# Performance work log

Hardware: AMD Instinct MI355X
Metric: run time of the kernel (lower is better)

Reference implementation:

```python
import jax, jax.numpy as jnp
import numpy as np
import math
from jax import lax

B, C, L = 8, 512, 1024
NCONV, K, H = 4, 7, 8
DH = C // H
EPS = 1e-5
NEG = -1e30


def layer_norm(x, g, b):
    mu = jnp.mean(x, axis=-1, keepdims=True)
    var = jnp.mean(jnp.square(x - mu), axis=-1, keepdims=True)
    return (x - mu) * lax.rsqrt(var + EPS) * g + b


def positional_encoding(d, n):
    pos = jnp.arange(n, dtype=jnp.float32)[:, None]                     # [n,1]
    div = jnp.exp(jnp.arange(0, d, 2, dtype=jnp.float32) * (-math.log(10000.0) / d))
    ang = pos * div                                                      # [n,d/2]
    pe = jnp.zeros((d, n), dtype=jnp.float32)
    pe = pe.at[0::2].set(jnp.sin(ang).T).at[1::2].set(jnp.cos(ang).T)
    return pe                                                            # [d,n]


def setup_inputs() -> dict:
    key = jax.random.key(0)
    ks = jax.random.split(key, 20)
    s = 0.02
    inp = {
        "x": jax.random.normal(ks[0], (B, C, L), jnp.float32),
        "mask": jnp.ones((B, L), jnp.float32),
        # conv stack params (stacked over NCONV layers)
        "dw_w": jax.random.normal(ks[1], (NCONV, C, 1, K), jnp.float32) * s,
        "dw_b": jnp.zeros((NCONV, C), jnp.float32),
        "pw_w": jax.random.normal(ks[2], (NCONV, C, C), jnp.float32) * s,
        "pw_b": jnp.zeros((NCONV, C), jnp.float32),
        "ln_conv_g": jnp.ones((NCONV, C), jnp.float32),
        "ln_conv_b": jnp.zeros((NCONV, C), jnp.float32),
        # attention params (torch Linear layout: [out,in])
        "Wq": jax.random.normal(ks[3], (C, C), jnp.float32) * s,
        "bq": jnp.zeros((C,), jnp.float32),
        "Wk": jax.random.normal(ks[4], (C, C), jnp.float32) * s,
        "bk": jnp.zeros((C,), jnp.float32),
        "Wv": jax.random.normal(ks[5], (C, C), jnp.float32) * s,
        "bv": jnp.zeros((C,), jnp.float32),
        "Wo": jax.random.normal(ks[6], (C, C), jnp.float32) * s,
        "bo": jnp.zeros((C,), jnp.float32),
        "ln_att_g": jnp.ones((C,), jnp.float32),
        "ln_att_b": jnp.zeros((C,), jnp.float32),
        # final fc + its layernorm
        "Wf": jax.random.normal(ks[7], (C, C), jnp.float32) * s,
        "bf": jnp.zeros((C,), jnp.float32),
        "ln_fc_g": jnp.ones((C,), jnp.float32),
        "ln_fc_b": jnp.zeros((C,), jnp.float32),
    }
    return inp


def reference(x, mask, dw_w, dw_b, pw_w, pw_b, ln_conv_g, ln_conv_b,
              Wq, bq, Wk, bk, Wv, bv, Wo, bo, ln_att_g, ln_att_b,
              Wf, bf, ln_fc_g, ln_fc_b):
    # positional encoding on channels-first input, then -> [B,L,C]
    out = x + positional_encoding(C, L)[None]          # [B,C,L]; dropout = eval mode (identity)
    out = out.transpose(0, 2, 1)                       # [B,L,C]
    res = out
    for i in range(NCONV):                             # fixed small layer loop
        h = layer_norm(out, ln_conv_g[i], ln_conv_b[i])
        h = h.transpose(0, 2, 1)                       # [B,C,L]
        h = lax.conv_general_dilated(h, dw_w[i], (1,), [(K // 2, K // 2)],
                                     dimension_numbers=("NCH", "OIH", "NCH"),
                                     feature_group_count=C) + dw_b[i][None, :, None]
        h = jnp.einsum("bcl,oc->bol", h, pw_w[i]) + pw_b[i][None, :, None]
        h = jax.nn.relu(h).transpose(0, 2, 1)          # [B,L,C]
        out = h + res
        res = out
    # masked multi-head self-attention
    a = layer_norm(out, ln_att_g, ln_att_b)
    q = (a @ Wq.T + bq).reshape(B, L, H, DH)
    k = (a @ Wk.T + bk).reshape(B, L, H, DH)
    v = (a @ Wv.T + bv).reshape(B, L, H, DH)
    scale = 1.0 / math.sqrt(DH)
    scores = jnp.einsum("blhd,bmhd->bhlm", q, k) * scale   # [B,H,L,L]
    m = mask[:, None, None, :]                              # mask over keys
    scores = scores * m + (1.0 - m) * NEG
    attn = jax.nn.softmax(scores, axis=-1)
    o = jnp.einsum("bhlm,bmhd->blhd", attn, v).reshape(B, L, C)
    o = o @ Wo.T + bo
    out = o + res
    res = out
    # feed-forward (single Linear + relu) with residual
    f = layer_norm(out, ln_fc_g, ln_fc_b)
    f = jax.nn.relu(f @ Wf.T + bf)
    out = f + res
    return out
```

## Files before the change

### kernel.cpp

```cpp
#include <hip/hip_runtime.h>
#include <hip/hip_bf16.h>

#define L_SEQ 1024
#define CCH   512
#define NB    8

typedef __bf16 bf16_t;
typedef __bf16 bf16x4 __attribute__((ext_vector_type(4)));
typedef __bf16 bf16x8 __attribute__((ext_vector_type(8)));
typedef float  f32x4  __attribute__((ext_vector_type(4)));

__device__ __forceinline__ void gload_lds16(const void* g, void* l) {
  __builtin_amdgcn_global_load_lds((const __attribute__((address_space(1))) void*)g,
                                   (__attribute__((address_space(3))) void*)l, 16, 0, 0);
}

__global__ __launch_bounds__(256) void prep_kernel(
    const float* __restrict__ x,
    const float* __restrict__ pw_w, const float* __restrict__ Wq,
    const float* __restrict__ Wk, const float* __restrict__ Wv,
    const float* __restrict__ Wo, const float* __restrict__ Wf,
    const float* __restrict__ dw_w,
    bf16_t* __restrict__ WPW, bf16_t* __restrict__ WQKV,
    bf16_t* __restrict__ WOB, bf16_t* __restrict__ WFB,
    float* __restrict__ WT,
    bf16_t* __restrict__ out, float* __restrict__ Psum, float* __restrict__ Psq) {
  int blk = blockIdx.x;
  if (blk < 4096) {
    __shared__ float tile[32][33];
    int bx = blk & 31, by = (blk >> 5) & 15, b = blk >> 9;
    int l0 = bx * 32, c0 = by * 32;
    int tx = threadIdx.x & 31, ty = threadIdx.x >> 5;
#pragma unroll
    for (int r = 0; r < 32; r += 8)
      tile[ty + r][tx] = x[(size_t)(b * CCH + c0 + ty + r) * L_SEQ + l0 + tx];
    __syncthreads();
#pragma unroll
    for (int r = 0; r < 32; r += 8) {
      int l = l0 + ty + r, c = c0 + tx;
      float div = expf(-(float)(2 * (c >> 1)) * (9.210340371976184f / 512.0f));
      float ang = (float)l * div;
      float pe = (c & 1) ? cosf(ang) : sinf(ang);
      float v = tile[tx][ty + r] + pe;
      out[(size_t)(b * L_SEQ + l) * CCH + c] = (bf16_t)v;
      float s = v, q = v * v;
#pragma unroll
      for (int off = 1; off < 32; off <<= 1) {
        s += __shfl_xor(s, off);
        q += __shfl_xor(q, off);
      }
      if (tx == 0) {
        size_t row = (size_t)(b * L_SEQ + l);
        Psum[row * 16 + (c0 >> 5)] = s;
        Psq[row * 16 + (c0 >> 5)] = q;
      }
    }
    return;
  }
  int idx = (blk - 4096) * 256 + threadIdx.x;
  if (idx < 1048576) { WPW[idx] = (bf16_t)pw_w[idx]; return; }
  idx -= 1048576;
  if (idx < 262144) { WQKV[idx] = (bf16_t)Wq[idx]; return; }
  idx -= 262144;
  if (idx < 262144) { WQKV[262144 + idx] = (bf16_t)Wk[idx]; return; }
  idx -= 262144;
  if (idx < 262144) { WQKV[524288 + idx] = (bf16_t)Wv[idx]; return; }
  idx -= 262144;
  if (idx < 262144) { WOB[idx] = (bf16_t)Wo[idx]; return; }
  idx -= 262144;
  if (idx < 262144) { WFB[idx] = (bf16_t)Wf[idx]; return; }
  idx -= 262144;
  if (idx < 14336) {
    int i = idx / 3584, r = idx % 3584, t = r >> 9, c = r & 511;
    WT[idx] = dw_w[i * 3584 + c * 7 + t];
  }
}

__global__ __launch_bounds__(256) void ln_apply_kernel(const bf16_t* __restrict__ in,
                                                       const float* __restrict__ Psum,
                                                       const float* __restrict__ Psq,
                                                       const float* __restrict__ gam,
                                                       const float* __restrict__ bet,
                                                       bf16_t* __restrict__ out) {
  int w = threadIdx.x >> 6, l = threadIdx.x & 63;
  int row = blockIdx.x * 4 + w;
  float v0 = 0.f;
  if (l < 16) v0 = Psum[(size_t)row * 16 + l];
  else if (l < 32) v0 = Psq[(size_t)row * 16 + (l - 16)];
  v0 += __shfl_xor(v0, 1); v0 += __shfl_xor(v0, 2);
  v0 += __shfl_xor(v0, 4); v0 += __shfl_xor(v0, 8);
  float sum = __shfl(v0, 0), sq = __shfl(v0, 16);
  float mean = sum * (1.0f / 512.0f);
  float var = sq * (1.0f / 512.0f) - mean * mean;
  float inv = rsqrtf(var + 1e-5f);
  bf16x8 hv = *(const bf16x8*)(in + (size_t)row * CCH + l * 8);
  float gv[8], bv[8];
  *(float4*)(&gv[0]) = *(const float4*)(gam + l * 8);
  *(float4*)(&gv[4]) = *(const float4*)(gam + l * 8 + 4);
  *(float4*)(&bv[0]) = *(const float4*)(bet + l * 8);
  *(float4*)(&bv[4]) = *(const float4*)(bet + l * 8 + 4);
  bf16x8 o;
#pragma unroll
  for (int j = 0; j < 8; j++) o[j] = (bf16_t)(((float)hv[j] - mean) * inv * gv[j] + bv[j]);
  *(bf16x8*)(out + (size_t)row * CCH + l * 8) = o;
}

__global__ __launch_bounds__(256) void dwln_kernel(const bf16_t* __restrict__ in,
                                                   const float* __restrict__ Psum,
                                                   const float* __restrict__ Psq,
                                                   const float* __restrict__ gam,
                                                   const float* __restrict__ bet,
                                                   const float* __restrict__ wtt,
                                                   const float* __restrict__ dbias,
                                                   bf16_t* __restrict__ out) {
  int idx = blockIdx.x * 256 + threadIdx.x;
  int lane = threadIdx.x & 63;
  int row = idx >> 6;
  int l = row & (L_SEQ - 1);
  float m_ = 0.f, i_ = 0.f;
  if (lane < 7) {
    int ll = l + lane - 3;
    if (ll >= 0 && ll < L_SEQ) {
      int rr = row + lane - 3;
      float s = 0.f, q = 0.f;
#pragma unroll
      for (int c = 0; c < 16; c++) { s += Psum[(size_t)rr * 16 + c]; q += Psq[(size_t)rr * 16 + c]; }
      float mm = s * (1.0f / 512.0f);
      m_ = mm;
      i_ = rsqrtf(q * (1.0f / 512.0f) - mm * mm + 1e-5f);
    }
  }
  float gv[8], bv[8], acc[8];
  *(float4*)&gv[0] = *(const float4*)(gam + lane * 8);
  *(float4*)&gv[4] = *(const float4*)(gam + lane * 8 + 4);
  *(float4*)&bv[0] = *(const float4*)(bet + lane * 8);
  *(float4*)&bv[4] = *(const float4*)(bet + lane * 8 + 4);
  *(float4*)&acc[0] = *(const float4*)(dbias + lane * 8);
  *(float4*)&acc[4] = *(const float4*)(dbias + lane * 8 + 4);
#pragma unroll
  for (int t = 0; t < 7; t++) {
    float mt = __shfl(m_, t), it = __shfl(i_, t);
    int ll = l + t - 3;
    if (ll >= 0 && ll < L_SEQ) {
      bf16x8 hv = *(const bf16x8*)(in + (size_t)(row + t - 3) * CCH + lane * 8);
      float wv[8];
      *(float4*)&wv[0] = *(const float4*)(wtt + t * CCH + lane * 8);
      *(float4*)&wv[4] = *(const float4*)(wtt + t * CCH + lane * 8 + 4);
#pragma unroll
      for (int j = 0; j < 8; j++)
        acc[j] += (((float)hv[j] - mt) * it * gv[j] + bv[j]) * wv[j];
    }
  }
  bf16x8 o;
#pragma unroll
  for (int j = 0; j < 8; j++) o[j] = (bf16_t)acc[j];
  *(bf16x8*)&out[(size_t)row * CCH + lane * 8] = o;
}

#define GSTAGE64(SRCA, SRCB, BI, K0)                                              \
  do {                                                                            \
    _Pragma("unroll") for (int cc = 0; cc < 2; cc++) {                            \
      int row_ = cc * 32 + w * 8 + srow;                                          \
      int off_ = (scb ^ ((row_ & 7) << 4)) >> 1;                                  \
      gload_lds16(SRCA + (size_t)(m0 + row_) * CCH + (K0) + off_,                 \
                  &As[BI][(cc * 32 + w * 8) * 64]);                               \
    }                                                                             \
    _Pragma("unroll") for (int cc = 0; cc < 4; cc++) {                            \
      int row_ = cc * 32 + w * 8 + srow;                                          \
      int off_ = (scb ^ ((row_ & 7) << 4)) >> 1;                                  \
      gload_lds16(SRCB + (size_t)(n0 + row_) * CCH + (K0) + off_,                 \
                  &Bs[BI][(cc * 32 + w * 8) * 64]);                               \
    }                                                                             \
  } while (0)

#define GCOMP64(BI)                                                               \
  do {                                                                            \
    __builtin_amdgcn_s_setprio(1);                                                \
    _Pragma("unroll") for (int ks = 0; ks < 2; ks++) {                            \
      bf16x8 fa[2], fb[4];                                                        \
      _Pragma("unroll") for (int i = 0; i < 2; i++) {                             \
        int ra = wr * 32 + i * 16 + lc;                                           \
        fa[i] = *(const bf16x8*)&As[BI][ra * 64 +                                 \
                 (((ks * 64 + lg * 16) ^ ((ra & 7) << 4)) >> 1)];                 \
      }                                                                           \
      _Pragma("unroll") for (int j = 0; j < 4; j++) {                             \
        int rb = wc * 64 + j * 16 + lc;                                           \
        fb[j] = *(const bf16x8*)&Bs[BI][rb * 64 +                                 \
                 (((ks * 64 + lg * 16) ^ ((rb & 7) << 4)) >> 1)];                 \
      }                                                                           \
      _Pragma("unroll") for (int i = 0; i < 2; i++)                               \
        _Pragma("unroll") for (int j = 0; j < 4; j++)                             \
          acc[i][j] = __builtin_amdgcn_mfma_f32_16x16x32_bf16(fa[i], fb[j],       \
                                                              acc[i][j], 0, 0, 0);\
    }                                                                             \
    __builtin_amdgcn_s_setprio(0);                                                \
  } while (0)

template <int RELU, int RES, int OUTF32, int STATS>
__global__ __launch_bounds__(256) void gemm_kernel(const bf16_t* __restrict__ A,
                                                   const bf16_t* __restrict__ W,
                                                   const float* __restrict__ bias,
                                                   const bf16_t* __restrict__ res,
                                                   float* __restrict__ outf,
                                                   bf16_t* __restrict__ outb,
                                                   float* __restrict__ Psum,
                                                   float* __restrict__ Psq) {
  __shared__ __align__(16) bf16_t As[2][64 * 64];
  __shared__ __align__(16) bf16_t Bs[2][128 * 64];
  int tid = threadIdx.x;
  int w = tid >> 6, l = tid & 63;
  int m0 = blockIdx.x * 64, n0 = blockIdx.y * 128;
  int wr = w >> 1, wc = w & 1;
  int lc = l & 15, lg = l >> 4;
  int srow = l >> 3, scb = (l & 7) * 16;
  f32x4 acc[2][4];
#pragma unroll
  for (int i = 0; i < 2; i++)
#pragma unroll
    for (int j = 0; j < 4; j++) acc[i][j] = f32x4{0.f, 0.f, 0.f, 0.f};

  GSTAGE64(A, W, 0, 0);
  __syncthreads();
  int cur = 0;
  for (int t = 0; t < 8; t++) {
    if (t < 7) GSTAGE64(A, W, cur ^ 1, (t + 1) * 64);
    GCOMP64(cur);
    __syncthreads();
    cur ^= 1;
  }

#pragma unroll
  for (int i = 0; i < 2; i++) {
    int mbase = m0 + wr * 32 + i * 16 + lg * 4;
    float ps[2][4], pq[2][4];
    if (STATS) {
#pragma unroll
      for (int jh = 0; jh < 2; jh++)
#pragma unroll
        for (int r = 0; r < 4; r++) { ps[jh][r] = 0.f; pq[jh][r] = 0.f; }
    }
#pragma unroll
    for (int j = 0; j < 4; j++) {
      int n = n0 + wc * 64 + j * 16 + lc;
      float bn = bias[n];
#pragma unroll
      for (int r = 0; r < 4; r++) {
        int m = mbase + r;
        float v2 = acc[i][j][r] + bn;
        if (RELU) v2 = fmaxf(v2, 0.f);
        if (RES) v2 += (float)res[(size_t)m * CCH + n];
        if (OUTF32) outf[(size_t)m * CCH + n] = v2;
        else outb[(size_t)m * CCH + n] = (bf16_t)v2;
        if (STATS) { ps[j >> 1][r] += v2; pq[j >> 1][r] += v2 * v2; }
      }
    }
    if (STATS) {
#pragma unroll
      for (int jh = 0; jh < 2; jh++)
#pragma unroll
        for (int r = 0; r < 4; r++) {
          float s = ps[jh][r], q = pq[jh][r];
          s += __shfl_xor(s, 1); q += __shfl_xor(q, 1);
          s += __shfl_xor(s, 2); q += __shfl_xor(q, 2);
          s += __shfl_xor(s, 4); q += __shfl_xor(q, 4);
          s += __shfl_xor(s, 8); q += __shfl_xor(q, 8);
          if (lc == 0) {
            size_t row = mbase + r;
            Psum[row * 16 + blockIdx.y * 4 + wc * 2 + jh] = s;
            Psq[row * 16 + blockIdx.y * 4 + wc * 2 + jh] = q;
          }
        }
    }
  }
}

#define GEMM_STAGE(SRCA, SRCB, BI, K0)                                            \
  do {                                                                            \
    {                                                                             \
      int row_ = w * 8 + srow;                                                    \
      int off_ = (scb ^ ((row_ & 7) << 4)) >> 1;                                  \
      gload_lds16(SRCA + (size_t)(m0 + row_) * CCH + (K0) + off_,                 \
                  &As[BI][(w * 8) * 64]);                                         \
    }                                                                             \
    _Pragma("unroll") for (int cc = 0; cc < 8; cc++) {                            \
      int row_ = cc * 32 + w * 8 + srow;                                          \
      int off_ = (scb ^ ((row_ & 7) << 4)) >> 1;                                  \
      gload_lds16(SRCB + (size_t)(n0 + row_) * CCH + (K0) + off_,                 \
                  &Bs[BI][(cc * 32 + w * 8) * 64]);                               \
    }                                                                             \
  } while (0)

#define GEMM_COMPUTE(BI)                                                          \
  do {                                                                            \
    __builtin_amdgcn_s_setprio(1);                                                \
    _Pragma("unroll") for (int ks = 0; ks < 2; ks++) {                            \
      bf16x8 fa[2], fb[4];                                                        \
      _Pragma("unroll") for (int i = 0; i < 2; i++) {                             \
        int ra = i * 16 + lc;                                                     \
        fa[i] = *(const bf16x8*)&As[BI][ra * 64 +                                 \
                 (((ks * 64 + lg * 16) ^ ((ra & 7) << 4)) >> 1)];                 \
      }                                                                           \
      _Pragma("unroll") for (int j = 0; j < 4; j++) {                             \
        int rb = w * 64 + j * 16 + lc;                                            \
        fb[j] = *(const bf16x8*)&Bs[BI][rb * 64 +                                 \
                 (((ks * 64 + lg * 16) ^ ((rb & 7) << 4)) >> 1)];                 \
      }                                                                           \
      _Pragma("unroll") for (int i = 0; i < 2; i++)                               \
        _Pragma("unroll") for (int j = 0; j < 4; j++)                             \
          acc[i][j] = __builtin_amdgcn_mfma_f32_16x16x32_bf16(fa[i], fb[j],       \
                                                              acc[i][j], 0, 0, 0);\
    }                                                                             \
    __builtin_amdgcn_s_setprio(0);                                                \
  } while (0)

__global__ __launch_bounds__(256) void qkv_kernel(const bf16_t* __restrict__ A,
                                                  const bf16_t* __restrict__ Wqkv,
                                                  const float* __restrict__ bq,
                                                  const float* __restrict__ bk,
                                                  const float* __restrict__ bv,
                                                  bf16_t* __restrict__ QB,
                                                  bf16_t* __restrict__ KB,
                                                  bf16_t* __restrict__ VT) {
  __shared__ __align__(16) bf16_t As[2][32 * 64];
  __shared__ __align__(16) bf16_t Bs[2][256 * 64];
  int tid = threadIdx.x;
  int w = tid >> 6, l = tid & 63;
  int m0 = blockIdx.x * 32, n0 = blockIdx.y * 256;
  int sec = n0 >> 9;
  int lc = l & 15, lg = l >> 4;
  int srow = l >> 3, scb = (l & 7) * 16;
  f32x4 acc[2][4];
#pragma unroll
  for (int i = 0; i < 2; i++)
#pragma unroll
    for (int j = 0; j < 4; j++) acc[i][j] = f32x4{0.f, 0.f, 0.f, 0.f};

  GEMM_STAGE(A, Wqkv, 0, 0);
  __syncthreads();
  int cur = 0;
  for (int t = 0; t < 8; t++) {
    if (t < 7) GEMM_STAGE(A, Wqkv, cur ^ 1, (t + 1) * 64);
    GEMM_COMPUTE(cur);
    __syncthreads();
    cur ^= 1;
  }

  const float* bp = (sec == 0) ? bq : (sec == 1) ? bk : bv;
#pragma unroll
  for (int i = 0; i < 2; i++) {
    int mbase = m0 + i * 16 + lg * 4;
#pragma unroll
    for (int j = 0; j < 4; j++) {
      int n = n0 + w * 64 + j * 16 + lc;
      int nl = n & 511;
      float bn = bp[nl];
      if (sec < 2) {
        bf16_t* ob = (sec == 0) ? QB : KB;
#pragma unroll
        for (int r = 0; r < 4; r++)
          ob[(size_t)(mbase + r) * CCH + nl] = (bf16_t)(acc[i][j][r] + bn);
      } else {
        int h = nl >> 6, d = nl & 63;
        int b = mbase >> 10, lpos = mbase & 1023;
        bf16x4 t;
#pragma unroll
        for (int r = 0; r < 4; r++) t[r] = (bf16_t)(acc[i][j][r] + bn);
        *(bf16x4*)&VT[(((size_t)(b * 8 + h) * 64 + d) * L_SEQ) + lpos] = t;
      }
    }
  }
}

#define ATT_STAGE(BI, KC)                                                         \
  do {                                                                            \
    _Pragma("unroll") for (int r = 0; r < 2; r++) {                               \
      int row = r * 32 + w * 8 + srow;                                            \
      int sc = (scb ^ ((row & 7) << 4)) >> 1;                                     \
      int key = (KC) * 64 + row;                                                  \
      gload_lds16(K + ((size_t)(b * L_SEQ + key) * CCH + h * 64 + sc),            \
                  &Ks[BI][(r * 32 + w * 8) * 64]);                                \
      gload_lds16(VT + (((size_t)(b * 8 + h) * 64 + row) * L_SEQ + (KC) * 64 + sc),\
                  &Vs[BI][(r * 32 + w * 8) * 64]);                                \
    }                                                                             \
  } while (0)

__global__ __launch_bounds__(256) void attn_kernel(const bf16_t* __restrict__ Q,
                                                   const bf16_t* __restrict__ K,
                                                   const bf16_t* __restrict__ VT,
                                                   const float* __restrict__ mask,
                                                   bf16_t* __restrict__ O) {
  __shared__ __align__(16) bf16_t Ks[2][64 * 64];
  __shared__ __align__(16) bf16_t Vs[2][64 * 64];
  __shared__ __align__(16) bf16_t Pl[4][16 * 64];
  int tid = threadIdx.x;
  int w = tid >> 6, l = tid & 63;
  int bid = blockIdx.x;
  int sw = (bid & 7) * 64 + (bid >> 3);
  int qb = sw & 7, h = (sw >> 3) & 7, b = sw >> 6;
  int lg = l >> 4, lc = l & 15;

  bf16x8 qf[2][2];
#pragma unroll
  for (int s = 0; s < 2; s++) {
    int qrow = qb * 128 + s * 64 + w * 16 + lc;
    const bf16_t* qptr = Q + ((size_t)(b * L_SEQ + qrow) * CCH + h * 64);
    qf[s][0] = *(const bf16x8*)(qptr + lg * 8);
    qf[s][1] = *(const bf16x8*)(qptr + 32 + lg * 8);
  }

  f32x4 oacc[2][4];
  float psl[2][4];
#pragma unroll
  for (int s = 0; s < 2; s++)
#pragma unroll
    for (int nf = 0; nf < 4; nf++) {
      oacc[s][nf] = f32x4{0.f, 0.f, 0.f, 0.f};
      psl[s][nf] = 0.f;
    }

  int srow = l >> 3;
  int scb = (l & 7) * 16;

  ATT_STAGE(0, 0);
  __syncthreads();
  int cur = 0;
  for (int kc = 0; kc < 16; kc++) {
    if (kc < 15) ATT_STAGE(cur ^ 1, kc + 1);

    float mv[4];
#pragma unroll
    for (int kf = 0; kf < 4; kf++) mv[kf] = mask[b * L_SEQ + kc * 64 + kf * 16 + lc];

#pragma unroll
    for (int s = 0; s < 2; s++) {
      f32x4 sacc[4];
#pragma unroll
      for (int kf = 0; kf < 4; kf++) sacc[kf] = f32x4{0.f, 0.f, 0.f, 0.f};
      __builtin_amdgcn_s_setprio(1);
#pragma unroll
      for (int kf = 0; kf < 4; kf++) {
        int row = kf * 16 + lc;
        int sx = (row & 7) << 4;
        const bf16_t* kr = &Ks[cur][row * 64];
        bf16x8 b0 = *(const bf16x8*)(kr + (((lg * 16) ^ sx) >> 1));
        sacc[kf] = __builtin_amdgcn_mfma_f32_16x16x32_bf16(qf[s][0], b0, sacc[kf], 0, 0, 0);
        bf16x8 b1 = *(const bf16x8*)(kr + (((64 + lg * 16) ^ sx) >> 1));
        sacc[kf] = __builtin_amdgcn_mfma_f32_16x16x32_bf16(qf[s][1], b1, sacc[kf], 0, 0, 0);
      }
      __builtin_amdgcn_s_setprio(0);

#pragma unroll
      for (int kf = 0; kf < 4; kf++) {
        float mneg = (1.f - mv[kf]) * (-1e30f);
        float msc = 0.125f * mv[kf];
#pragma unroll
        for (int j = 0; j < 4; j++) {
          float p = __expf(sacc[kf][j] * msc + mneg);
          psl[s][j] += p;
          int q = lg * 4 + j;
          int cb = (kf * 32 + lc * 2) ^ ((q & 7) << 4);
          Pl[w][(q * 128 + cb) >> 1] = (bf16_t)p;
        }
      }

      int sp = (lc & 7) << 4;
      bf16x8 pa0 = *(const bf16x8*)&Pl[w][(lc * 128 + ((lg * 16) ^ sp)) >> 1];
      bf16x8 pa1 = *(const bf16x8*)&Pl[w][(lc * 128 + ((64 + lg * 16) ^ sp)) >> 1];
      __builtin_amdgcn_s_setprio(1);
#pragma unroll
      for (int nf = 0; nf < 4; nf++) {
        int d = nf * 16 + lc;
        int sx = (d & 7) << 4;
        const bf16_t* vr = &Vs[cur][d * 64];
        bf16x8 vb0 = *(const bf16x8*)(vr + (((lg * 16) ^ sx) >> 1));
        oacc[s][nf] = __builtin_amdgcn_mfma_f32_16x16x32_bf16(pa0, vb0, oacc[s][nf], 0, 0, 0);
        bf16x8 vb1 = *(const bf16x8*)(vr + (((64 + lg * 16) ^ sx) >> 1));
        oacc[s][nf] = __builtin_amdgcn_mfma_f32_16x16x32_bf16(pa1, vb1, oacc[s][nf], 0, 0, 0);
      }
      __builtin_amdgcn_s_setprio(0);
    }
    __syncthreads();
    cur ^= 1;
  }

#pragma unroll
  for (int off = 1; off < 16; off <<= 1)
#pragma unroll
    for (int s = 0; s < 2; s++)
#pragma unroll
      for (int j = 0; j < 4; j++) psl[s][j] += __shfl_xor(psl[s][j], off);

#pragma unroll
  for (int s = 0; s < 2; s++)
#pragma unroll
    for (int j = 0; j < 4; j++) {
      float is = 1.0f / psl[s][j];
      int r = qb * 128 + s * 64 + w * 16 + lg * 4 + j;
      bf16_t* op = O + ((size_t)(b * L_SEQ + r) * CCH + h * 64);
#pragma unroll
      for (int nf = 0; nf < 4; nf++) op[nf * 16 + lc] = (bf16_t)(oacc[s][nf][j] * is);
    }
}

extern "C" void kernel_launch(void* const* d_in, const int* in_sizes, int n_in,
                              void* d_out, int out_size, void* d_ws, size_t ws_size,
                              hipStream_t stream) {
  const float* x = (const float*)d_in[0];
  const float* mask = (const float*)d_in[1];
  const float* dw_w = (const float*)d_in[2];
  const float* dw_b = (const float*)d_in[3];
  const float* pw_w = (const float*)d_in[4];
  const float* pw_b = (const float*)d_in[5];
  const float* ln_conv_g = (const float*)d_in[6];
  const float* ln_conv_b = (const float*)d_in[7];
  const float* Wq = (const float*)d_in[8];  const float* bq = (const float*)d_in[9];
  const float* Wk = (const float*)d_in[10]; const float* bk = (const float*)d_in[11];
  const float* Wv = (const float*)d_in[12]; const float* bv = (const float*)d_in[13];
  const float* Wo = (const float*)d_in[14]; const float* bo = (const float*)d_in[15];
  const float* ln_att_g = (const float*)d_in[16]; const float* ln_att_b = (const float*)d_in[17];
  const float* Wf = (const float*)d_in[18]; const float* bfc = (const float*)d_in[19];
  const float* ln_fc_g = (const float*)d_in[20]; const float* ln_fc_b = (const float*)d_in[21];

  char* ws = (char*)d_ws;
  bf16_t* ABF  = (bf16_t*)(ws);
  bf16_t* QB   = (bf16_t*)(ws + (8u << 20));
  bf16_t* KB   = (bf16_t*)(ws + (16u << 20));
  bf16_t* VT   = (bf16_t*)(ws + (24u << 20));
  char*   wb   = ws + (32u << 20);
  bf16_t* WPW  = (bf16_t*)(wb);
  bf16_t* WQKV = (bf16_t*)(wb + (2u << 20));
  bf16_t* WOB  = (bf16_t*)(wb + 3584u * 1024);
  bf16_t* WFB  = (bf16_t*)(wb + (4u << 20));
  float*  WT   = (float*)(wb + 4608u * 1024);
  float*  Psum = (float*)(ws + (38u << 20));
  float*  Psq  = (float*)(ws + (38u << 20) + 524288);
  bf16_t* OUT  = (bf16_t*)(ws + (40u << 20));

  prep_kernel<<<15416, 256, 0, stream>>>(x, pw_w, Wq, Wk, Wv, Wo, Wf, dw_w,
                                         WPW, WQKV, WOB, WFB, WT,
                                         OUT, Psum, Psq);

  dim3 ggrid(128, 4);
  for (int i = 0; i < 4; i++) {
    dwln_kernel<<<2048, 256, 0, stream>>>(OUT, Psum, Psq, ln_conv_g + i * 512,
                                          ln_conv_b + i * 512, WT + i * 3584,
                                          dw_b + i * 512, ABF);
    gemm_kernel<1, 1, 0, 1><<<ggrid, 256, 0, stream>>>(ABF, WPW + i * 262144,
                                                       pw_b + i * 512, OUT,
                                                       nullptr, OUT, Psum, Psq);
  }
  ln_apply_kernel<<<2048, 256, 0, stream>>>(OUT, Psum, Psq, ln_att_g, ln_att_b, ABF);
  qkv_kernel<<<dim3(256, 6), 256, 0, stream>>>(ABF, WQKV, bq, bk, bv, QB, KB, VT);
  attn_kernel<<<512, 256, 0, stream>>>(QB, KB, VT, mask, ABF);
  gemm_kernel<0, 1, 0, 1><<<ggrid, 256, 0, stream>>>(ABF, WOB, bo, OUT,
                                                     nullptr, OUT, Psum, Psq);
  ln_apply_kernel<<<2048, 256, 0, stream>>>(OUT, Psum, Psq, ln_fc_g, ln_fc_b, ABF);
  gemm_kernel<1, 1, 1, 0><<<ggrid, 256, 0, stream>>>(ABF, WFB, bfc, OUT,
                                                     (float*)d_out, nullptr,
                                                     nullptr, nullptr);
}
```

Measured before the change: 334.3 us.

## Fuse layernorm and depthwise conv into GEMM A-tile producers, ping-pong buffers

Removes the standalone dwln and ln_apply kernels. The layernorm (and, for the conv stack, the 7-tap depthwise conv) is now computed while staging the A tile inside the pointwise, QKV and FC GEMMs. Because a GEMM can no longer read and write the same buffer in place, activations and row statistics ping-pong between two buffers. This saves several kernel launches and a full bf16 write and read of the activation per layer. In exchange, the A-side work is recomputed once per N-tile block (4 or 6 times), and the conv path needs 14 register-held row loads per thread, which raises register pressure.

```diff
diff --git a/kernel.cpp b/kernel.cpp
--- a/kernel.cpp
+++ b/kernel.cpp
@@ -4,6 +4,7 @@
 #define L_SEQ 1024
 #define CCH   512
 #define NB    8
+#define NROW  (NB * L_SEQ)
 
 typedef __bf16 bf16_t;
 typedef __bf16 bf16x4 __attribute__((ext_vector_type(4)));
@@ -75,103 +76,6 @@
     WT[idx] = dw_w[i * 3584 + c * 7 + t];
   }
 }
-
-__global__ __launch_bounds__(256) void ln_apply_kernel(const bf16_t* __restrict__ in,
-                                                       const float* __restrict__ Psum,
-                                                       const float* __restrict__ Psq,
-                                                       const float* __restrict__ gam,
-                                                       const float* __restrict__ bet,
-                                                       bf16_t* __restrict__ out) {
-  int w = threadIdx.x >> 6, l = threadIdx.x & 63;
-  int row = blockIdx.x * 4 + w;
-  float v0 = 0.f;
-  if (l < 16) v0 = Psum[(size_t)row * 16 + l];
-  else if (l < 32) v0 = Psq[(size_t)row * 16 + (l - 16)];
-  v0 += __shfl_xor(v0, 1); v0 += __shfl_xor(v0, 2);
-  v0 += __shfl_xor(v0, 4); v0 += __shfl_xor(v0, 8);
-  float sum = __shfl(v0, 0), sq = __shfl(v0, 16);
-  float mean = sum * (1.0f / 512.0f);
-  float var = sq * (1.0f / 512.0f) - mean * mean;
-  float inv = rsqrtf(var + 1e-5f);
-  bf16x8 hv = *(const bf16x8*)(in + (size_t)row * CCH + l * 8);
-  float gv[8], bv[8];
-  *(float4*)(&gv[0]) = *(const float4*)(gam + l * 8);
-  *(float4*)(&gv[4]) = *(const float4*)(gam + l * 8 + 4);
-  *(float4*)(&bv[0]) = *(const float4*)(bet + l * 8);
-  *(float4*)(&bv[4]) = *(const float4*)(bet + l * 8 + 4);
-  bf16x8 o;
-#pragma unroll
-  for (int j = 0; j < 8; j++) o[j] = (bf16_t)(((float)hv[j] - mean) * inv * gv[j] + bv[j]);
-  *(bf16x8*)(out + (size_t)row * CCH + l * 8) = o;
-}
-
-__global__ __launch_bounds__(256) void dwln_kernel(const bf16_t* __restrict__ in,
-                                                   const float* __restrict__ Psum,
-                                                   const float* __restrict__ Psq,
-                                                   const float* __restrict__ gam,
-                                                   const float* __restrict__ bet,
-                                                   const float* __restrict__ wtt,
-                                                   const float* __restrict__ dbias,
-                                                   bf16_t* __restrict__ out) {
-  int idx = blockIdx.x * 256 + threadIdx.x;
-  int lane = threadIdx.x & 63;
-  int row = idx >> 6;
-  int l = row & (L_SEQ - 1);
-  float m_ = 0.f, i_ = 0.f;
-  if (lane < 7) {
-    int ll = l + lane - 3;
-    if (ll >= 0 && ll < L_SEQ) {
-      int rr = row + lane - 3;
-      float s = 0.f, q = 0.f;
-#pragma unroll
-      for (int c = 0; c < 16; c++) { s += Psum[(size_t)rr * 16 + c]; q += Psq[(size_t)rr * 16 + c]; }
-      float mm = s * (1.0f / 512.0f);
-      m_ = mm;
-      i_ = rsqrtf(q * (1.0f / 512.0f) - mm * mm + 1e-5f);
-    }
-  }
-  float gv[8], bv[8], acc[8];
-  *(float4*)&gv[0] = *(const float4*)(gam + lane * 8);
-  *(float4*)&gv[4] = *(const float4*)(gam + lane * 8 + 4);
-  *(float4*)&bv[0] = *(const float4*)(bet + lane * 8);
-  *(float4*)&bv[4] = *(const float4*)(bet + lane * 8 + 4);
-  *(float4*)&acc[0] = *(const float4*)(dbias + lane * 8);
-  *(float4*)&acc[4] = *(const float4*)(dbias + lane * 8 + 4);
-#pragma unroll
-  for (int t = 0; t < 7; t++) {
-    float mt = __shfl(m_, t), it = __shfl(i_, t);
-    int ll = l + t - 3;
-    if (ll >= 0 && ll < L_SEQ) {
-      bf16x8 hv = *(const bf16x8*)(in + (size_t)(row + t - 3) * CCH + lane * 8);
-      float wv[8];
-      *(float4*)&wv[0] = *(const float4*)(wtt + t * CCH + lane * 8);
-      *(float4*)&wv[4] = *(const float4*)(wtt + t * CCH + lane * 8 + 4);
-#pragma unroll
-      for (int j = 0; j < 8; j++)
-        acc[j] += (((float)hv[j] - mt) * it * gv[j] + bv[j]) * wv[j];
-    }
-  }
-  bf16x8 o;
-#pragma unroll
-  for (int j = 0; j < 8; j++) o[j] = (bf16_t)acc[j];
-  *(bf16x8*)&out[(size_t)row * CCH + lane * 8] = o;
-}
-
-#define GSTAGE64(SRCA, SRCB, BI, K0)                                              \
-  do {                                                                            \
-    _Pragma("unroll") for (int cc = 0; cc < 2; cc++) {                            \
-      int row_ = cc * 32 + w * 8 + srow;                                          \
-      int off_ = (scb ^ ((row_ & 7) << 4)) >> 1;                                  \
-      gload_lds16(SRCA + (size_t)(m0 + row_) * CCH + (K0) + off_,                 \
-                  &As[BI][(cc * 32 + w * 8) * 64]);                               \
-    }                                                                             \
-    _Pragma("unroll") for (int cc = 0; cc < 4; cc++) {                            \
-      int row_ = cc * 32 + w * 8 + srow;                                          \
-      int off_ = (scb ^ ((row_ & 7) << 4)) >> 1;                                  \
-      gload_lds16(SRCB + (size_t)(n0 + row_) * CCH + (K0) + off_,                 \
-                  &Bs[BI][(cc * 32 + w * 8) * 64]);                               \
-    }                                                                             \
-  } while (0)
 
 #define GCOMP64(BI)                                                               \
   do {                                                                            \
@@ -196,15 +100,168 @@
     __builtin_amdgcn_s_setprio(0);                                                \
   } while (0)
 
-template <int RELU, int RES, int OUTF32, int STATS>
-__global__ __launch_bounds__(256) void gemm_kernel(const bf16_t* __restrict__ A,
-                                                   const bf16_t* __restrict__ W,
-                                                   const float* __restrict__ bias,
-                                                   const bf16_t* __restrict__ res,
-                                                   float* __restrict__ outf,
-                                                   bf16_t* __restrict__ outb,
-                                                   float* __restrict__ Psum,
-                                                   float* __restrict__ Psq) {
+#define BSTAGE128(SRCB, BI, K0)                                                   \
+  _Pragma("unroll") for (int cc = 0; cc < 4; cc++) {                              \
+    int row_ = cc * 32 + w * 8 + srow;                                            \
+    int off_ = (scb ^ ((row_ & 7) << 4)) >> 1;                                    \
+    gload_lds16(SRCB + (size_t)(n0 + row_) * CCH + (K0) + off_,                   \
+                &Bs[BI][(cc * 32 + w * 8) * 64]);                                 \
+  }
+
+__global__ __launch_bounds__(256) void gemm_conv(
+    const bf16_t* __restrict__ IN, const float* __restrict__ Psum,
+    const float* __restrict__ Psq,
+    const float* __restrict__ gam, const float* __restrict__ bet,
+    const float* __restrict__ wtt, const float* __restrict__ dbias,
+    const bf16_t* __restrict__ W, const float* __restrict__ bias,
+    bf16_t* __restrict__ OUTn, float* __restrict__ PsumO,
+    float* __restrict__ PsqO) {
+  __shared__ __align__(16) bf16_t As[2][64 * 64];
+  __shared__ __align__(16) bf16_t Bs[2][128 * 64];
+  __shared__ float2 st[72];
+  int tid = threadIdx.x;
+  int w = tid >> 6, l = tid & 63;
+  int m0 = blockIdx.x * 64, n0 = blockIdx.y * 128;
+  int wr = w >> 1, wc = w & 1;
+  int lc = l & 15, lg = l >> 4;
+  int srow = l >> 3, scb = (l & 7) * 16;
+  int cl = (l & 7) * 8;
+
+  if (tid < 70) {
+    int gr = m0 - 3 + tid;
+    float s = 0.f, q = 0.f;
+    if (gr >= 0 && gr < NROW) {
+#pragma unroll
+      for (int c = 0; c < 16; c++) {
+        s += Psum[(size_t)gr * 16 + c];
+        q += Psq[(size_t)gr * 16 + c];
+      }
+    }
+    float mean = s * (1.f / 512.f);
+    float inv = rsqrtf(q * (1.f / 512.f) - mean * mean + 1e-5f);
+    st[tid] = make_float2(mean, inv);
+  }
+  __syncthreads();
+
+  int row0 = w * 8 + srow, row1 = row0 + 32;
+  int csw = (scb ^ ((row0 & 7) << 4)) >> 1;
+  int gl0 = (m0 + row0) & (L_SEQ - 1);
+  int gl1 = (m0 + row1) & (L_SEQ - 1);
+  float2 mi0[7], mi1[7];
+  bool v0[7], v1[7];
+#pragma unroll
+  for (int t = 0; t < 7; t++) {
+    mi0[t] = st[row0 + t];
+    mi1[t] = st[row1 + t];
+    v0[t] = (unsigned)(gl0 + t - 3) < L_SEQ;
+    v1[t] = (unsigned)(gl1 + t - 3) < L_SEQ;
+  }
+
+  bf16x8 hv0[7], hv1[7];
+#define CONV_ALOAD(K0)                                                            \
+  _Pragma("unroll") for (int t = 0; t < 7; t++) {                                 \
+    int r0_ = m0 + row0 + t - 3; r0_ = r0_ < 0 ? 0 : (r0_ > NROW - 1 ? NROW - 1 : r0_); \
+    int r1_ = m0 + row1 + t - 3; r1_ = r1_ < 0 ? 0 : (r1_ > NROW - 1 ? NROW - 1 : r1_); \
+    hv0[t] = *(const bf16x8*)&IN[(size_t)r0_ * CCH + (K0) + cl];                  \
+    hv1[t] = *(const bf16x8*)&IN[(size_t)r1_ * CCH + (K0) + cl];                  \
+  }
+
+#define CONV_AWRITE(BI, K0)                                                       \
+  do {                                                                            \
+    float gv[8], bv[8], a0[8], a1[8];                                             \
+    *(float4*)&gv[0] = *(const float4*)(gam + (K0) + cl);                         \
+    *(float4*)&gv[4] = *(const float4*)(gam + (K0) + cl + 4);                     \
+    *(float4*)&bv[0] = *(const float4*)(bet + (K0) + cl);                         \
+    *(float4*)&bv[4] = *(const float4*)(bet + (K0) + cl + 4);                     \
+    *(float4*)&a0[0] = *(const float4*)(dbias + (K0) + cl);                       \
+    *(float4*)&a0[4] = *(const float4*)(dbias + (K0) + cl + 4);                   \
+    _Pragma("unroll") for (int j = 0; j < 8; j++) a1[j] = a0[j];                  \
+    _Pragma("unroll") for (int t = 0; t < 7; t++) {                               \
+      float wv[8];                                                                \
+      *(float4*)&wv[0] = *(const float4*)(wtt + t * CCH + (K0) + cl);             \
+      *(float4*)&wv[4] = *(const float4*)(wtt + t * CCH + (K0) + cl + 4);         \
+      if (v0[t]) {                                                                \
+        _Pragma("unroll") for (int j = 0; j < 8; j++)                             \
+          a0[j] += (((float)hv0[t][j] - mi0[t].x) * mi0[t].y * gv[j] + bv[j]) * wv[j]; \
+      }                                                                           \
+      if (v1[t]) {                                                                \
+        _Pragma("unroll") for (int j = 0; j < 8; j++)                             \
+          a1[j] += (((float)hv1[t][j] - mi1[t].x) * mi1[t].y * gv[j] + bv[j]) * wv[j]; \
+      }                                                                           \
+    }                                                                             \
+    bf16x8 o0, o1;                                                                \
+    _Pragma("unroll") for (int j = 0; j < 8; j++) {                               \
+      o0[j] = (bf16_t)a0[j]; o1[j] = (bf16_t)a1[j];                               \
+    }                                                                             \
+    *(bf16x8*)&As[BI][row0 * 64 + csw] = o0;                                      \
+    *(bf16x8*)&As[BI][row1 * 64 + csw] = o1;                                      \
+  } while (0)
+
+  f32x4 acc[2][4];
+#pragma unroll
+  for (int i = 0; i < 2; i++)
+#pragma unroll
+    for (int j = 0; j < 4; j++) acc[i][j] = f32x4{0.f, 0.f, 0.f, 0.f};
+
+  BSTAGE128(W, 0, 0);
+  CONV_ALOAD(0);
+  CONV_AWRITE(0, 0);
+  __syncthreads();
+  int cur = 0;
+  for (int kk = 0; kk < 8; kk++) {
+    if (kk < 7) { BSTAGE128(W, cur ^ 1, (kk + 1) * 64); CONV_ALOAD((kk + 1) * 64); }
+    GCOMP64(cur);
+    if (kk < 7) CONV_AWRITE(cur ^ 1, (kk + 1) * 64);
+    __syncthreads();
+    cur ^= 1;
+  }
+
+#pragma unroll
+  for (int i = 0; i < 2; i++) {
+    int mbase = m0 + wr * 32 + i * 16 + lg * 4;
+    float ps[2][4], pq[2][4];
+#pragma unroll
+    for (int jh = 0; jh < 2; jh++)
+#pragma unroll
+      for (int r = 0; r < 4; r++) { ps[jh][r] = 0.f; pq[jh][r] = 0.f; }
+#pragma unroll
+    for (int j = 0; j < 4; j++) {
+      int n = n0 + wc * 64 + j * 16 + lc;
+      float bn = bias[n];
+#pragma unroll
+      for (int r = 0; r < 4; r++) {
+        int m = mbase + r;
+        float v2 = fmaxf(acc[i][j][r] + bn, 0.f) + (float)IN[(size_t)m * CCH + n];
+        OUTn[(size_t)m * CCH + n] = (bf16_t)v2;
+        ps[j >> 1][r] += v2;
+        pq[j >> 1][r] += v2 * v2;
+      }
+    }
+#pragma unroll
+    for (int jh = 0; jh < 2; jh++)
+#pragma unroll
+      for (int r = 0; r < 4; r++) {
+        float s = ps[jh][r], q = pq[jh][r];
+        s += __shfl_xor(s, 1); q += __shfl_xor(q, 1);
+        s += __shfl_xor(s, 2); q += __shfl_xor(q, 2);
+        s += __shfl_xor(s, 4); q += __shfl_xor(q, 4);
+        s += __shfl_xor(s, 8); q += __shfl_xor(q, 8);
+        if (lc == 0) {
+          size_t row = mbase + r;
+          PsumO[row * 16 + blockIdx.y * 4 + wc * 2 + jh] = s;
+          PsqO[row * 16 + blockIdx.y * 4 + wc * 2 + jh] = q;
+        }
+      }
+  }
+}
+
+__global__ __launch_bounds__(256) void gemm_wo(const bf16_t* __restrict__ A,
+                                               const bf16_t* __restrict__ W,
+                                               const float* __restrict__ bias,
+                                               const bf16_t* __restrict__ res,
+                                               bf16_t* __restrict__ outb,
+                                               float* __restrict__ PsumO,
+                                               float* __restrict__ PsqO) {
   __shared__ __align__(16) bf16_t As[2][64 * 64];
   __shared__ __align__(16) bf16_t Bs[2][128 * 64];
   int tid = threadIdx.x;
@@ -219,11 +276,20 @@
 #pragma unroll
     for (int j = 0; j < 4; j++) acc[i][j] = f32x4{0.f, 0.f, 0.f, 0.f};
 
-  GSTAGE64(A, W, 0, 0);
+#define WO_ASTAGE(BI, K0)                                                         \
+  _Pragma("unroll") for (int cc = 0; cc < 2; cc++) {                              \
+    int row_ = cc * 32 + w * 8 + srow;                                            \
+    int off_ = (scb ^ ((row_ & 7) << 4)) >> 1;                                    \
+    gload_lds16(A + (size_t)(m0 + row_) * CCH + (K0) + off_,                      \
+                &As[BI][(cc * 32 + w * 8) * 64]);                                 \
+  }
+
+  WO_ASTAGE(0, 0);
+  BSTAGE128(W, 0, 0);
   __syncthreads();
   int cur = 0;
-  for (int t = 0; t < 8; t++) {
-    if (t < 7) GSTAGE64(A, W, cur ^ 1, (t + 1) * 64);
+  for (int kk = 0; kk < 8; kk++) {
+    if (kk < 7) { WO_ASTAGE(cur ^ 1, (kk + 1) * 64); BSTAGE128(W, cur ^ 1, (kk + 1) * 64); }
     GCOMP64(cur);
     __syncthreads();
     cur ^= 1;
@@ -233,12 +299,10 @@
   for (int i = 0; i < 2; i++) {
     int mbase = m0 + wr * 32 + i * 16 + lg * 4;
     float ps[2][4], pq[2][4];
-    if (STATS) {
-#pragma unroll
-      for (int jh = 0; jh < 2; jh++)
-#pragma unroll
-        for (int r = 0; r < 4; r++) { ps[jh][r] = 0.f; pq[jh][r] = 0.f; }
-    }
+#pragma unroll
+    for (int jh = 0; jh < 2; jh++)
+#pragma unroll
+      for (int r = 0; r < 4; r++) { ps[jh][r] = 0.f; pq[jh][r] = 0.f; }
 #pragma unroll
     for (int j = 0; j < 4; j++) {
       int n = n0 + wc * 64 + j * 16 + lc;
@@ -246,74 +310,131 @@
 #pragma unroll
       for (int r = 0; r < 4; r++) {
         int m = mbase + r;
-        float v2 = acc[i][j][r] + bn;
-        if (RELU) v2 = fmaxf(v2, 0.f);
-        if (RES) v2 += (float)res[(size_t)m * CCH + n];
-        if (OUTF32) outf[(size_t)m * CCH + n] = v2;
-        else outb[(size_t)m * CCH + n] = (bf16_t)v2;
-        if (STATS) { ps[j >> 1][r] += v2; pq[j >> 1][r] += v2 * v2; }
-      }
-    }
-    if (STATS) {
-#pragma unroll
-      for (int jh = 0; jh < 2; jh++)
-#pragma unroll
-        for (int r = 0; r < 4; r++) {
-          float s = ps[jh][r], q = pq[jh][r];
-          s += __shfl_xor(s, 1); q += __shfl_xor(q, 1);
-          s += __shfl_xor(s, 2); q += __shfl_xor(q, 2);
-          s += __shfl_xor(s, 4); q += __shfl_xor(q, 4);
-          s += __shfl_xor(s, 8); q += __shfl_xor(q, 8);
-          if (lc == 0) {
-            size_t row = mbase + r;
-            Psum[row * 16 + blockIdx.y * 4 + wc * 2 + jh] = s;
-            Psq[row * 16 + blockIdx.y * 4 + wc * 2 + jh] = q;
-          }
+        float v2 = acc[i][j][r] + bn + (float)res[(size_t)m * CCH + n];
+        outb[(size_t)m * CCH + n] = (bf16_t)v2;
+        ps[j >> 1][r] += v2;
+        pq[j >> 1][r] += v2 * v2;
+      }
+    }
+#pragma unroll
+    for (int jh = 0; jh < 2; jh++)
+#pragma unroll
+      for (int r = 0; r < 4; r++) {
+        float s = ps[jh][r], q = pq[jh][r];
+        s += __shfl_xor(s, 1); q += __shfl_xor(q, 1);
+        s += __shfl_xor(s, 2); q += __shfl_xor(q, 2);
+        s += __shfl_xor(s, 4); q += __shfl_xor(q, 4);
+        s += __shfl_xor(s, 8); q += __shfl_xor(q, 8);
+        if (lc == 0) {
+          size_t row = mbase + r;
+          PsumO[row * 16 + blockIdx.y * 4 + wc * 2 + jh] = s;
+          PsqO[row * 16 + blockIdx.y * 4 + wc * 2 + jh] = q;
         }
-    }
+      }
   }
 }
 
-#define GEMM_STAGE(SRCA, SRCB, BI, K0)                                            \
+__global__ __launch_bounds__(256) void gemm_fc(const bf16_t* __restrict__ IN,
+                                               const float* __restrict__ Psum,
+                                               const float* __restrict__ Psq,
+                                               const float* __restrict__ gam,
+                                               const float* __restrict__ bet,
+                                               const bf16_t* __restrict__ W,
+                                               const float* __restrict__ bias,
+                                               float* __restrict__ outf) {
+  __shared__ __align__(16) bf16_t As[2][64 * 64];
+  __shared__ __align__(16) bf16_t Bs[2][128 * 64];
+  __shared__ float2 st[64];
+  int tid = threadIdx.x;
+  int w = tid >> 6, l = tid & 63;
+  int m0 = blockIdx.x * 64, n0 = blockIdx.y * 128;
+  int wr = w >> 1, wc = w & 1;
+  int lc = l & 15, lg = l >> 4;
+  int srow = l >> 3, scb = (l & 7) * 16;
+  int cl = (l & 7) * 8;
+
+  if (tid < 64) {
+    int gr = m0 + tid;
+    float s = 0.f, q = 0.f;
+#pragma unroll
+    for (int c = 0; c < 16; c++) {
+      s += Psum[(size_t)gr * 16 + c];
+      q += Psq[(size_t)gr * 16 + c];
+    }
+    float mean = s * (1.f / 512.f);
+    float inv = rsqrtf(q * (1.f / 512.f) - mean * mean + 1e-5f);
+    st[tid] = make_float2(mean, inv);
+  }
+  __syncthreads();
+
+  int row0 = w * 8 + srow, row1 = row0 + 32;
+  int csw = (scb ^ ((row0 & 7) << 4)) >> 1;
+  float2 mi0 = st[row0], mi1 = st[row1];
+  bf16x8 h0, h1;
+
+#define FC_ALOAD(K0)                                                              \
   do {                                                                            \
-    {                                                                             \
-      int row_ = w * 8 + srow;                                                    \
-      int off_ = (scb ^ ((row_ & 7) << 4)) >> 1;                                  \
-      gload_lds16(SRCA + (size_t)(m0 + row_) * CCH + (K0) + off_,                 \
-                  &As[BI][(w * 8) * 64]);                                         \
+    h0 = *(const bf16x8*)&IN[(size_t)(m0 + row0) * CCH + (K0) + cl];              \
+    h1 = *(const bf16x8*)&IN[(size_t)(m0 + row1) * CCH + (K0) + cl];              \
+  } while (0)
+
+#define FC_AWRITE(BI, K0)                                                         \
+  do {                                                                            \
+    float gv[8], bv[8];                                                           \
+    *(float4*)&gv[0] = *(const float4*)(gam + (K0) + cl);                         \
+    *(float4*)&gv[4] = *(const float4*)(gam + (K0) + cl + 4);                     \
+    *(float4*)&bv[0] = *(const float4*)(bet + (K0) + cl);                         \
+    *(float4*)&bv[4] = *(const float4*)(bet + (K0) + cl + 4);                     \
+    bf16x8 o0, o1;                                                                \
+    _Pragma("unroll") for (int j = 0; j < 8; j++) {                               \
+      o0[j] = (bf16_t)(((float)h0[j] - mi0.x) * mi0.y * gv[j] + bv[j]);           \
+      o1[j] = (bf16_t)(((float)h1[j] - mi1.x) * mi1.y * gv[j] + bv[j]);           \
     }                                                                             \
-    _Pragma("unroll") for (int cc = 0; cc < 8; cc++) {                            \
-      int row_ = cc * 32 + w * 8 + srow;                                          \
-      int off_ = (scb ^ ((row_ & 7) << 4)) >> 1;                                  \
-      gload_lds16(SRCB + (size_t)(n0 + row_) * CCH + (K0) + off_,                 \
-                  &Bs[BI][(cc * 32 + w * 8) * 64]);                               \
-    }                                                                             \
+    *(bf16x8*)&As[BI][row0 * 64 + csw] = o0;                                      \
+    *(bf16x8*)&As[BI][row1 * 64 + csw] = o1;                                      \
   } while (0)
 
-#define GEMM_COMPUTE(BI)                                                          \
-  do {                                                                            \
-    __builtin_amdgcn_s_setprio(1);                                                \
-    _Pragma("unroll") for (int ks = 0; ks < 2; ks++) {                            \
-      bf16x8 fa[2], fb[4];                                                        \
-      _Pragma("unroll") for (int i = 0; i < 2; i++) {                             \
-        int ra = i * 16 + lc;                                                     \
-        fa[i] = *(const bf16x8*)&As[BI][ra * 64 +                                 \
-                 (((ks * 64 + lg * 16) ^ ((ra & 7) << 4)) >> 1)];                 \
-      }                                                                           \
-      _Pragma("unroll") for (int j = 0; j < 4; j++) {                             \
-        int rb = w * 64 + j * 16 + lc;                                            \
-        fb[j] = *(const bf16x8*)&Bs[BI][rb * 64 +                                 \
-                 (((ks * 64 + lg * 16) ^ ((rb & 7) << 4)) >> 1)];                 \
-      }                                                                           \
-      _Pragma("unroll") for (int i = 0; i < 2; i++)                               \
-        _Pragma("unroll") for (int j = 0; j < 4; j++)                             \
-          acc[i][j] = __builtin_amdgcn_mfma_f32_16x16x32_bf16(fa[i], fb[j],       \
-                                                              acc[i][j], 0, 0, 0);\
-    }                                                                             \
-    __builtin_amdgcn_s_setprio(0);                                                \
-  } while (0)
-
-__global__ __launch_bounds__(256) void qkv_kernel(const bf16_t* __restrict__ A,
+  f32x4 acc[2][4];
+#pragma unroll
+  for (int i = 0; i < 2; i++)
+#pragma unroll
+    for (int j = 0; j < 4; j++) acc[i][j] = f32x4{0.f, 0.f, 0.f, 0.f};
+
+  BSTAGE128(W, 0, 0);
+  FC_ALOAD(0);
+  FC_AWRITE(0, 0);
+  __syncthreads();
+  int cur = 0;
+  for (int kk = 0; kk < 8; kk++) {
+    if (kk < 7) { BSTAGE128(W, cur ^ 1, (kk + 1) * 64); FC_ALOAD((kk + 1) * 64); }
+    GCOMP64(cur);
+    if (kk < 7) FC_AWRITE(cur ^ 1, (kk + 1) * 64);
+    __syncthreads();
+    cur ^= 1;
+  }
+
+#pragma unroll
+  for (int i = 0; i < 2; i++) {
+    int mbase = m0 + wr * 32 + i * 16 + lg * 4;
+#pragma unroll
+    for (int j = 0; j < 4; j++) {
+      int n = n0 + wc * 64 + j * 16 + lc;
+      float bn = bias[n];
+#pragma unroll
+      for (int r = 0; r < 4; r++) {
+        int m = mbase + r;
+        float v2 = fmaxf(acc[i][j][r] + bn, 0.f) + (float)IN[(size_t)m * CCH + n];
+        outf[(size_t)m * CCH + n] = v2;
+      }
+    }
+  }
+}
+
+__global__ __launch_bounds__(256) void qkv_kernel(const bf16_t* __restrict__ IN,
+                                                  const float* __restrict__ Psum,
+                                                  const float* __restrict__ Psq,
+                                                  const float* __restrict__ gam,
+                                                  const float* __restrict__ bet,
                                                   const bf16_t* __restrict__ Wqkv,
                                                   const float* __restrict__ bq,
                                                   const float* __restrict__ bk,
@@ -323,24 +444,94 @@
                                                   bf16_t* __restrict__ VT) {
   __shared__ __align__(16) bf16_t As[2][32 * 64];
   __shared__ __align__(16) bf16_t Bs[2][256 * 64];
+  __shared__ float2 st[32];
   int tid = threadIdx.x;
   int w = tid >> 6, l = tid & 63;
   int m0 = blockIdx.x * 32, n0 = blockIdx.y * 256;
   int sec = n0 >> 9;
   int lc = l & 15, lg = l >> 4;
   int srow = l >> 3, scb = (l & 7) * 16;
+  int cl = (l & 7) * 8;
+
+  if (tid < 32) {
+    int gr = m0 + tid;
+    float s = 0.f, q = 0.f;
+#pragma unroll
+    for (int c = 0; c < 16; c++) {
+      s += Psum[(size_t)gr * 16 + c];
+      q += Psq[(size_t)gr * 16 + c];
+    }
+    float mean = s * (1.f / 512.f);
+    float inv = rsqrtf(q * (1.f / 512.f) - mean * mean + 1e-5f);
+    st[tid] = make_float2(mean, inv);
+  }
+  __syncthreads();
+
+  int row0 = w * 8 + srow;
+  int csw = (scb ^ ((row0 & 7) << 4)) >> 1;
+  float2 mi = st[row0];
+  bf16x8 hq;
+
+#define QKV_ALOAD(K0) hq = *(const bf16x8*)&IN[(size_t)(m0 + row0) * CCH + (K0) + cl]
+
+#define QKV_AWRITE(BI, K0)                                                        \
+  do {                                                                            \
+    float gv[8], bv[8];                                                           \
+    *(float4*)&gv[0] = *(const float4*)(gam + (K0) + cl);                         \
+    *(float4*)&gv[4] = *(const float4*)(gam + (K0) + cl + 4);                     \
+    *(float4*)&bv[0] = *(const float4*)(bet + (K0) + cl);                         \
+    *(float4*)&bv[4] = *(const float4*)(bet + (K0) + cl + 4);                     \
+    bf16x8 o;                                                                     \
+    _Pragma("unroll") for (int j = 0; j < 8; j++)                                 \
+      o[j] = (bf16_t)(((float)hq[j] - mi.x) * mi.y * gv[j] + bv[j]);              \
+    *(bf16x8*)&As[BI][row0 * 64 + csw] = o;                                       \
+  } while (0)
+
+#define QKV_BSTAGE(BI, K0)                                                        \
+  _Pragma("unroll") for (int cc = 0; cc < 8; cc++) {                              \
+    int row_ = cc * 32 + w * 8 + srow;                                            \
+    int off_ = (scb ^ ((row_ & 7) << 4)) >> 1;                                    \
+    gload_lds16(Wqkv + (size_t)(n0 + row_) * CCH + (K0) + off_,                   \
+                &Bs[BI][(cc * 32 + w * 8) * 64]);                                 \
+  }
+
   f32x4 acc[2][4];
 #pragma unroll
   for (int i = 0; i < 2; i++)
 #pragma unroll
     for (int j = 0; j < 4; j++) acc[i][j] = f32x4{0.f, 0.f, 0.f, 0.f};
 
-  GEMM_STAGE(A, Wqkv, 0, 0);
+  QKV_BSTAGE(0, 0);
+  QKV_ALOAD(0);
+  QKV_AWRITE(0, 0);
   __syncthreads();
   int cur = 0;
-  for (int t = 0; t < 8; t++) {
-    if (t < 7) GEMM_STAGE(A, Wqkv, cur ^ 1, (t + 1) * 64);
-    GEMM_COMPUTE(cur);
+  for (int kk = 0; kk < 8; kk++) {
+    if (kk < 7) { QKV_BSTAGE(cur ^ 1, (kk + 1) * 64); QKV_ALOAD((kk + 1) * 64); }
+    __builtin_amdgcn_s_setprio(1);
+#pragma unroll
+    for (int ks = 0; ks < 2; ks++) {
+      bf16x8 fa[2], fb[4];
+#pragma unroll
+      for (int i = 0; i < 2; i++) {
+        int ra = i * 16 + lc;
+        fa[i] = *(const bf16x8*)&As[cur][ra * 64 +
+                 (((ks * 64 + lg * 16) ^ ((ra & 7) << 4)) >> 1)];
+      }
+#pragma unroll
+      for (int j = 0; j < 4; j++) {
+        int rb = w * 64 + j * 16 + lc;
+        fb[j] = *(const bf16x8*)&Bs[cur][rb * 64 +
+                 (((ks * 64 + lg * 16) ^ ((rb & 7) << 4)) >> 1)];
+      }
+#pragma unroll
+      for (int i = 0; i < 2; i++)
+#pragma unroll
+        for (int j = 0; j < 4; j++)
+          acc[i][j] = __builtin_amdgcn_mfma_f32_16x16x32_bf16(fa[i], fb[j], acc[i][j], 0, 0, 0);
+    }
+    __builtin_amdgcn_s_setprio(0);
+    if (kk < 7) QKV_AWRITE(cur ^ 1, (kk + 1) * 64);
     __syncthreads();
     cur ^= 1;
   }
@@ -532,30 +723,32 @@
   bf16_t* WOB  = (bf16_t*)(wb + 3584u * 1024);
   bf16_t* WFB  = (bf16_t*)(wb + (4u << 20));
   float*  WT   = (float*)(wb + 4608u * 1024);
-  float*  Psum = (float*)(ws + (38u << 20));
-  float*  Psq  = (float*)(ws + (38u << 20) + 524288);
-  bf16_t* OUT  = (bf16_t*)(ws + (40u << 20));
+  float*  PsA  = (float*)(ws + (38u << 20));
+  float*  PsAq = PsA + 131072;
+  float*  PsB  = (float*)(ws + (39u << 20));
+  float*  PsBq = PsB + 131072;
+  bf16_t* OUTA = (bf16_t*)(ws + (40u << 20));
+  bf16_t* OUTB = (bf16_t*)(ws + (48u << 20));
 
   prep_kernel<<<15416, 256, 0, stream>>>(x, pw_w, Wq, Wk, Wv, Wo, Wf, dw_w,
                                          WPW, WQKV, WOB, WFB, WT,
-                                         OUT, Psum, Psq);
+                                         OUTA, PsA, PsAq);
 
   dim3 ggrid(128, 4);
+  bf16_t* ib[5] = {OUTA, OUTB, OUTA, OUTB, OUTA};
+  float*  ps[5] = {PsA, PsB, PsA, PsB, PsA};
+  float*  pq[5] = {PsAq, PsBq, PsAq, PsBq, PsAq};
   for (int i = 0; i < 4; i++) {
-    dwln_kernel<<<2048, 256, 0, stream>>>(OUT, Psum, Psq, ln_conv_g + i * 512,
-                                          ln_conv_b + i * 512, WT + i * 3584,
-                                          dw_b + i * 512, ABF);
-    gemm_kernel<1, 1, 0, 1><<<ggrid, 256, 0, stream>>>(ABF, WPW + i * 262144,
-                                                       pw_b + i * 512, OUT,
-                                                       nullptr, OUT, Psum, Psq);
-  }
-  ln_apply_kernel<<<2048, 256, 0, stream>>>(OUT, Psum, Psq, ln_att_g, ln_att_b, ABF);
-  qkv_kernel<<<dim3(256, 6), 256, 0, stream>>>(ABF, WQKV, bq, bk, bv, QB, KB, VT);
+    gemm_conv<<<ggrid, 256, 0, stream>>>(ib[i], ps[i], pq[i],
+                                         ln_conv_g + i * 512, ln_conv_b + i * 512,
+                                         WT + i * 3584, dw_b + i * 512,
+                                         WPW + i * 262144, pw_b + i * 512,
+                                         ib[i + 1], ps[i + 1], pq[i + 1]);
+  }
+  qkv_kernel<<<dim3(256, 6), 256, 0, stream>>>(OUTA, PsA, PsAq, ln_att_g, ln_att_b,
+                                               WQKV, bq, bk, bv, QB, KB, VT);
   attn_kernel<<<512, 256, 0, stream>>>(QB, KB, VT, mask, ABF);
-  gemm_kernel<0, 1, 0, 1><<<ggrid, 256, 0, stream>>>(ABF, WOB, bo, OUT,
-                                                     nullptr, OUT, Psum, Psq);
-  ln_apply_kernel<<<2048, 256, 0, stream>>>(OUT, Psum, Psq, ln_fc_g, ln_fc_b, ABF);
-  gemm_kernel<1, 1, 1, 0><<<ggrid, 256, 0, stream>>>(ABF, WFB, bfc, OUT,
-                                                     (float*)d_out, nullptr,
-                                                     nullptr, nullptr);
+  gemm_wo<<<ggrid, 256, 0, stream>>>(ABF, WOB, bo, OUTA, OUTB, PsB, PsBq);
+  gemm_fc<<<ggrid, 256, 0, stream>>>(OUTB, PsB, PsBq, ln_fc_g, ln_fc_b,
+                                     WFB, bfc, (float*)d_out);
 }
```

Result: slower. 472.9 us (+41.5%).
